# Kernel optimization log

Measured on AMD Instinct MI355X. Metric: run time of the kernel, lower is better.

The kernel has to match this reference:

```python
import jax, jax.numpy as jnp
import numpy as np

# TT-matrix dense layer: y = relu(x @ M + b) where M is a TT-matrix with cores
# G_k of shape [r_{k-1}, m_k, n_k, r_k], M[i1..id, j1..jd] = G1[:,i1,j1,:] ... Gd[:,id,jd,:]

IN_DIMS = [8, 8, 8, 8]
OUT_DIMS = [8, 8, 8, 8]
RANKS = [1, 8, 8, 8, 1]
BATCH = 4096


def setup_inputs() -> dict:
    key = jax.random.key(0)
    ks = jax.random.split(key, 6)
    inp = {"x": jax.random.normal(ks[0], (BATCH, int(np.prod(IN_DIMS))), dtype=jnp.float32)}
    # glorot-ish scale for TT cores so that the reconstructed matrix has sane variance
    for k in range(4):
        shape = (RANKS[k], IN_DIMS[k], OUT_DIMS[k], RANKS[k + 1])
        scale = 0.3
        inp[f"core{k}"] = scale * jax.random.normal(ks[1 + k], shape, dtype=jnp.float32)
    inp["b"] = 0.1 * jnp.ones((int(np.prod(OUT_DIMS)),), dtype=jnp.float32)
    return inp


def _tt_matmul(x, cores):
    # x: [B, prod(m)], cores[k]: [r_{k-1}, m_k, n_k, r_k]
    B = x.shape[0]
    ms = [G.shape[1] for G in cores]
    # res: [a, r, m_k, t] with a = B * prod(n_done), t = prod(m_rest)
    res = x.reshape(B, 1, ms[0], -1)
    for k, G in enumerate(cores):
        a, _, _, t = res.shape
        n, r_next = G.shape[2], G.shape[3]
        # contract rank and current input mode: [a, n, r_next, t]
        res = jnp.einsum('aqmt,qmnr->anrt', res, G)
        m_next = ms[k + 1] if k + 1 < len(cores) else 1
        res = res.reshape(a * n, r_next, m_next, t // m_next)
    return res.reshape(B, -1)  # [B, prod(n)], big-endian output index order


def reference(x, core0, core1, core2, core3, b):
    y = _tt_matmul(x, [core0, core1, core2, core3])
    return jax.nn.relu(y + b)
```

## Files before the change

### kernel.cpp

```cpp
#include <hip/hip_runtime.h>
#include <hip/hip_bf16.h>
#include <stdint.h>

typedef short bf16x8 __attribute__((ext_vector_type(8)));
typedef float f32x4 __attribute__((ext_vector_type(4)));
typedef unsigned short u16;
typedef u16 ushort8 __attribute__((ext_vector_type(8)));

typedef __attribute__((address_space(3))) void lds_void;
typedef const __attribute__((address_space(1))) void gbl_void;

#define BAR() do { asm volatile("" ::: "memory"); __builtin_amdgcn_s_barrier(); asm volatile("" ::: "memory"); } while (0)
#define WAITV(N) asm volatile("s_waitcnt vmcnt(" #N ")" ::: "memory")

__device__ __forceinline__ u16 f2bf(float f) {
  uint32_t u = __builtin_bit_cast(uint32_t, f);
  u += 0x7fffu + ((u >> 16) & 1u);
  return (u16)(u >> 16);
}

__global__ __launch_bounds__(256) void cvt_x(const float* __restrict__ x,
                                             u16* __restrict__ xb) {
  const int i = (blockIdx.x * 256 + threadIdx.x) * 8;
  float4 a = *(const float4*)(x + i);
  float4 b = *(const float4*)(x + i + 4);
  ushort8 o;
  o[0] = f2bf(a.x); o[1] = f2bf(a.y); o[2] = f2bf(a.z); o[3] = f2bf(a.w);
  o[4] = f2bf(b.x); o[5] = f2bf(b.y); o[6] = f2bf(b.z); o[7] = f2bf(b.w);
  *(ushort8*)(xb + i) = o;
}

__global__ __launch_bounds__(256) void build_mt(
    const float* __restrict__ c0, const float* __restrict__ c1,
    const float* __restrict__ c2, const float* __restrict__ c3,
    u16* __restrict__ Mt) {
  const int bid = blockIdx.x;
  const int j1 = bid & 7, i1 = (bid >> 3) & 7, j0 = (bid >> 6) & 7, i0 = bid >> 9;
  const int t = threadIdx.x;
  __shared__ float v[512];
  __shared__ float g3[512];
  g3[t] = c3[t];
  g3[t + 256] = c3[t + 256];
  float w2[8];
#pragma unroll
  for (int r2 = 0; r2 < 8; ++r2) {
    float s = 0.f;
#pragma unroll
    for (int r1 = 0; r1 < 8; ++r1)
      s += c0[(i0 * 8 + j0) * 8 + r1] * c1[((r1 * 8 + i1) * 8 + j1) * 8 + r2];
    w2[r2] = s;
  }
#pragma unroll
  for (int e = t; e < 512; e += 256) {
    const int r3 = e & 7, j2 = (e >> 3) & 7, i2 = e >> 6;
    float s = 0.f;
#pragma unroll
    for (int r2 = 0; r2 < 8; ++r2)
      s += w2[r2] * c2[((r2 * 8 + i2) * 8 + j2) * 8 + r3];
    v[e] = s;
  }
  __syncthreads();
  const int jr = t >> 2, ic0 = (t & 3) * 16;
  const int j2 = jr >> 3, j3 = jr & 7;
  const size_t base =
      (size_t)(j0 * 512 + j1 * 64 + jr) * 4096 + (i0 * 512 + i1 * 64) + ic0;
  ushort8 o0, o1;
#pragma unroll
  for (int q = 0; q < 16; ++q) {
    const int ic = ic0 + q, i2 = ic >> 3, i3 = ic & 7;
    float s = 0.f;
#pragma unroll
    for (int r3 = 0; r3 < 8; ++r3)
      s += v[(i2 << 6) + (j2 << 3) + r3] * g3[(r3 << 6) + (i3 << 3) + j3];
    const u16 h = f2bf(s);
    if (q < 8) o0[q] = h; else o1[q - 8] = h;
  }
  *(ushort8*)(Mt + base) = o0;
  *(ushort8*)(Mt + base + 8) = o1;
}

__global__ __launch_bounds__(512, 2) void gemm_bias_relu(
    const u16* __restrict__ A, const u16* __restrict__ Bt,
    const float* __restrict__ bias, float* __restrict__ C) {
  constexpr int K = 4096, N = 4096, NT = 64;
  __shared__ __align__(16) char lds[131072];
  const int t = threadIdx.x;
  const int l = t & 63, w = t >> 6;
  const int wr = w >> 2, wc = w & 3;
  const int lr = l & 15, lk = l >> 4;
  const int bm = blockIdx.y, bn = blockIdx.x;

  const char* gA = (const char*)A + (size_t)bm * 256 * (K * 2);
  const char* gB = (const char*)Bt + (size_t)bn * 256 * (K * 2);
  const int srow = t >> 3;
  const int schunk = (t & 7) ^ (srow & 7);
  const int sgo = srow * (K * 2) + schunk * 16;
  const int sld = t * 16;

  const int axor = (lk ^ (lr & 7)) * 16;
  const int aoff0 = (wr * 128 + lr) * 128 + axor;
  const int aoff1 = aoff0 ^ 64;
  const int boff0 = 65536 + (wc * 64 + lr) * 128 + axor;
  const int boff1 = boff0 ^ 64;

  auto stA = [&](int p, int h, int kt) {
    const char* src = gA + (size_t)(h * 128) * (K * 2) + kt * 128 + sgo;
    char* dst = lds + p * 32768 + h * 16384 + sld;
    __builtin_amdgcn_global_load_lds((gbl_void*)src, (lds_void*)dst, 16, 0, 0);
    __builtin_amdgcn_global_load_lds((gbl_void*)(src + (size_t)64 * (K * 2)),
                                     (lds_void*)(dst + 8192), 16, 0, 0);
  };
  auto stB = [&](int p, int h, int kt) {
    const char* src = gB + (size_t)(h * 128) * (K * 2) + kt * 128 + sgo;
    char* dst = lds + 65536 + p * 32768 + h * 16384 + sld;
    __builtin_amdgcn_global_load_lds((gbl_void*)src, (lds_void*)dst, 16, 0, 0);
    __builtin_amdgcn_global_load_lds((gbl_void*)(src + (size_t)64 * (K * 2)),
                                     (lds_void*)(dst + 8192), 16, 0, 0);
  };
  auto rdA = [&](int p, int off, int m) -> bf16x8 {
    return *(const bf16x8*)(lds + p * 32768 + off + m * 2048);
  };
  auto rdB = [&](int p, int off, int n) -> bf16x8 {
    return *(const bf16x8*)(lds + p * 32768 + off + n * 2048);
  };

  bf16x8 aH0[8], aH1[8], bH0[4], bH1[4];
  f32x4 acc[8][4];
#pragma unroll
  for (int m = 0; m < 8; ++m)
#pragma unroll
    for (int n = 0; n < 4; ++n) acc[m][n] = f32x4{0.f, 0.f, 0.f, 0.f};

  auto rdAH = [&](bf16x8* d, int p, int mh) {
#pragma unroll
    for (int m2 = 0; m2 < 4; ++m2) {
      d[m2 * 2 + 0] = rdA(p, aoff0, mh * 4 + m2);
      d[m2 * 2 + 1] = rdA(p, aoff1, mh * 4 + m2);
    }
  };
  auto rdBH = [&](bf16x8* d, int p, int nh) {
#pragma unroll
    for (int n2 = 0; n2 < 2; ++n2) {
      d[n2 * 2 + 0] = rdB(p, boff0, nh * 2 + n2);
      d[n2 * 2 + 1] = rdB(p, boff1, nh * 2 + n2);
    }
  };
  auto quad = [&](int mh, int nh, bf16x8* aH, bf16x8* bH) {
    __builtin_amdgcn_s_setprio(1);
#pragma unroll
    for (int kk = 0; kk < 2; ++kk)
#pragma unroll
      for (int m2 = 0; m2 < 4; ++m2)
#pragma unroll
        for (int n2 = 0; n2 < 2; ++n2)
          acc[mh * 4 + m2][nh * 2 + n2] = __builtin_amdgcn_mfma_f32_16x16x32_bf16(
              aH[m2 * 2 + kk], bH[n2 * 2 + kk], acc[mh * 4 + m2][nh * 2 + n2], 0, 0, 0);
    __builtin_amdgcn_s_setprio(0);
  };

  stA(0, 0, 0); stA(0, 1, 0); stB(0, 0, 0); stB(0, 1, 0);
  stB(1, 0, 1); stB(1, 1, 1);
  WAITV(4);
  BAR();
  rdAH(aH0, 0, 0); rdBH(bH0, 0, 0);
  stA(1, 0, 1);
  BAR();

  for (int it = 0; it < NT / 2; ++it) {
    const int T = 2 * it;
    const int t2 = (T + 2 < NT) ? T + 2 : NT - 1;
    const int t3 = (T + 3 < NT) ? T + 3 : NT - 1;
    rdBH(bH1, 0, 1);
    quad(0, 0, aH0, bH0);
    stA(1, 1, T + 1);
    BAR();
    rdAH(aH1, 0, 1);
    quad(0, 1, aH0, bH1);
    stB(0, 0, t2);
    BAR();
    quad(1, 1, aH1, bH1);
    stB(0, 1, t2); stA(0, 0, t2);
    WAITV(6);
    BAR();
    rdAH(aH0, 1, 0);
    quad(1, 0, aH1, bH0);
    rdBH(bH0, 1, 0);
    stA(0, 1, t2);
    BAR();
    rdBH(bH1, 1, 1);
    quad(0, 0, aH0, bH0);
    BAR();
    rdAH(aH1, 1, 1);
    quad(0, 1, aH0, bH1);
    stB(1, 0, t3);
    BAR();
    quad(1, 1, aH1, bH1);
    stB(1, 1, t3);
    WAITV(4);
    BAR();
    rdAH(aH0, 0, 0);
    quad(1, 0, aH1, bH0);
    rdBH(bH0, 0, 0);
    stA(1, 0, t3);
    BAR();
  }
  WAITV(0);

  const int row0 = bm * 256 + wr * 128;
  const int col0 = bn * 256 + wc * 64;
#pragma unroll
  for (int n = 0; n < 4; ++n) {
    const int col = col0 + n * 16 + lr;
    const float bv = bias[col];
#pragma unroll
    for (int m = 0; m < 8; ++m) {
      const int r0 = row0 + m * 16 + lk * 4;
#pragma unroll
      for (int vv = 0; vv < 4; ++vv) {
        const float val = acc[m][n][vv] + bv;
        C[(size_t)(r0 + vv) * N + col] = val > 0.f ? val : 0.f;
      }
    }
  }
}

extern "C" void kernel_launch(void* const* d_in, const int* in_sizes, int n_in,
                              void* d_out, int out_size, void* d_ws, size_t ws_size,
                              hipStream_t stream) {
  const float* x  = (const float*)d_in[0];
  const float* c0 = (const float*)d_in[1];
  const float* c1 = (const float*)d_in[2];
  const float* c2 = (const float*)d_in[3];
  const float* c3 = (const float*)d_in[4];
  const float* b  = (const float*)d_in[5];
  float* out = (float*)d_out;

  u16* xb  = (u16*)d_ws;
  u16* mtb = xb + (size_t)4096 * 4096;

  cvt_x<<<dim3(16777216 / (256 * 8)), dim3(256), 0, stream>>>(x, xb);
  build_mt<<<dim3(4096), dim3(256), 0, stream>>>(c0, c1, c2, c3, mtb);
  gemm_bias_relu<<<dim3(16, 16), dim3(512), 0, stream>>>(xb, mtb, b, out);
}
```

Baseline: 138.5 us.

## Fuse fp32-to-bf16 conversion of x into GEMM A-tile loading

Removes the separate cvt_x kernel and its bf16 staging buffer. The GEMM now loads fp32 rows of x into registers, converts them with v_cvt_pk_bf16_f32, and writes swizzled bf16 into LDS, so the A-tile pipeline is rescheduled around register-staged loads. The aim is to save a full kernel pass over x (read fp32, write bf16, reread) and one launch. In exchange the GEMM reads twice as many A bytes, needs extra registers (launch bounds drop to one block per CU), and adds more LDS waits in the main loop.

```diff
diff --git a/kernel.cpp b/kernel.cpp
--- a/kernel.cpp
+++ b/kernel.cpp
@@ -4,6 +4,7 @@
 
 typedef short bf16x8 __attribute__((ext_vector_type(8)));
 typedef float f32x4 __attribute__((ext_vector_type(4)));
+typedef float f32v4 __attribute__((ext_vector_type(4)));
 typedef unsigned short u16;
 typedef u16 ushort8 __attribute__((ext_vector_type(8)));
 
@@ -12,22 +13,12 @@
 
 #define BAR() do { asm volatile("" ::: "memory"); __builtin_amdgcn_s_barrier(); asm volatile("" ::: "memory"); } while (0)
 #define WAITV(N) asm volatile("s_waitcnt vmcnt(" #N ")" ::: "memory")
+#define LGKM0() asm volatile("s_waitcnt lgkmcnt(0)" ::: "memory")
 
 __device__ __forceinline__ u16 f2bf(float f) {
   uint32_t u = __builtin_bit_cast(uint32_t, f);
   u += 0x7fffu + ((u >> 16) & 1u);
   return (u16)(u >> 16);
-}
-
-__global__ __launch_bounds__(256) void cvt_x(const float* __restrict__ x,
-                                             u16* __restrict__ xb) {
-  const int i = (blockIdx.x * 256 + threadIdx.x) * 8;
-  float4 a = *(const float4*)(x + i);
-  float4 b = *(const float4*)(x + i + 4);
-  ushort8 o;
-  o[0] = f2bf(a.x); o[1] = f2bf(a.y); o[2] = f2bf(a.z); o[3] = f2bf(a.w);
-  o[4] = f2bf(b.x); o[5] = f2bf(b.y); o[6] = f2bf(b.z); o[7] = f2bf(b.w);
-  *(ushort8*)(xb + i) = o;
 }
 
 __global__ __launch_bounds__(256) void build_mt(
@@ -79,8 +70,8 @@
   *(ushort8*)(Mt + base + 8) = o1;
 }
 
-__global__ __launch_bounds__(512, 2) void gemm_bias_relu(
-    const u16* __restrict__ A, const u16* __restrict__ Bt,
+__global__ __launch_bounds__(512, 1) void gemm_bias_relu(
+    const float* __restrict__ X, const u16* __restrict__ Bt,
     const float* __restrict__ bias, float* __restrict__ C) {
   constexpr int K = 4096, N = 4096, NT = 64;
   __shared__ __align__(16) char lds[131072];
@@ -90,12 +81,14 @@
   const int lr = l & 15, lk = l >> 4;
   const int bm = blockIdx.y, bn = blockIdx.x;
 
-  const char* gA = (const char*)A + (size_t)bm * 256 * (K * 2);
+  const float* gAf = X + (size_t)bm * 256 * K;
   const char* gB = (const char*)Bt + (size_t)bn * 256 * (K * 2);
   const int srow = t >> 3;
   const int schunk = (t & 7) ^ (srow & 7);
   const int sgo = srow * (K * 2) + schunk * 16;
   const int sld = t * 16;
+  const int ar = t >> 2;
+  const int aq = t & 3;
 
   const int axor = (lk ^ (lr & 7)) * 16;
   const int aoff0 = (wr * 128 + lr) * 128 + axor;
@@ -103,12 +96,22 @@
   const int boff0 = 65536 + (wc * 64 + lr) * 128 + axor;
   const int boff1 = boff0 ^ 64;
 
-  auto stA = [&](int p, int h, int kt) {
-    const char* src = gA + (size_t)(h * 128) * (K * 2) + kt * 128 + sgo;
-    char* dst = lds + p * 32768 + h * 16384 + sld;
-    __builtin_amdgcn_global_load_lds((gbl_void*)src, (lds_void*)dst, 16, 0, 0);
-    __builtin_amdgcn_global_load_lds((gbl_void*)(src + (size_t)64 * (K * 2)),
-                                     (lds_void*)(dst + 8192), 16, 0, 0);
+  auto aload = [&](f32v4* L, int h, int kt) {
+    const float* src = gAf + (size_t)(h * 128 + ar) * K + kt * 64 + aq * 16;
+#pragma unroll
+    for (int j = 0; j < 4; ++j) L[j] = *(const f32v4*)(src + j * 4);
+  };
+  auto awrite = [&](const f32v4* L, int p, int h) {
+    uint32_t d[8];
+#pragma unroll
+    for (int j = 0; j < 4; ++j) {
+      asm("v_cvt_pk_bf16_f32 %0, %1, %2" : "=v"(d[2 * j]) : "v"(L[j][0]), "v"(L[j][1]));
+      asm("v_cvt_pk_bf16_f32 %0, %1, %2" : "=v"(d[2 * j + 1]) : "v"(L[j][2]), "v"(L[j][3]));
+    }
+    char* base = lds + p * 32768 + h * 16384 + ar * 128;
+    const int s = ar & 7;
+    *(uint4*)(base + (((2 * aq) ^ s) * 16)) = make_uint4(d[0], d[1], d[2], d[3]);
+    *(uint4*)(base + (((2 * aq + 1) ^ s) * 16)) = make_uint4(d[4], d[5], d[6], d[7]);
   };
   auto stB = [&](int p, int h, int kt) {
     const char* src = gB + (size_t)(h * 128) * (K * 2) + kt * 128 + sgo;
@@ -124,7 +127,7 @@
     return *(const bf16x8*)(lds + p * 32768 + off + n * 2048);
   };
 
-  bf16x8 aH0[8], aH1[8], bH0[4], bH1[4];
+  bf16x8 aH0[8], aH1[8], b01[2][2], b23[2][2];
   f32x4 acc[8][4];
 #pragma unroll
   for (int m = 0; m < 8; ++m)
@@ -138,14 +141,14 @@
       d[m2 * 2 + 1] = rdA(p, aoff1, mh * 4 + m2);
     }
   };
-  auto rdBH = [&](bf16x8* d, int p, int nh) {
+  auto rdBH = [&](bf16x8 (*d)[2], int p, int nh) {
 #pragma unroll
     for (int n2 = 0; n2 < 2; ++n2) {
-      d[n2 * 2 + 0] = rdB(p, boff0, nh * 2 + n2);
-      d[n2 * 2 + 1] = rdB(p, boff1, nh * 2 + n2);
-    }
-  };
-  auto quad = [&](int mh, int nh, bf16x8* aH, bf16x8* bH) {
+      d[n2][0] = rdB(p, boff0, nh * 2 + n2);
+      d[n2][1] = rdB(p, boff1, nh * 2 + n2);
+    }
+  };
+  auto quad = [&](int mh, int nh, bf16x8* aH, bf16x8 (*bH)[2]) {
     __builtin_amdgcn_s_setprio(1);
 #pragma unroll
     for (int kk = 0; kk < 2; ++kk)
@@ -154,54 +157,65 @@
 #pragma unroll
         for (int n2 = 0; n2 < 2; ++n2)
           acc[mh * 4 + m2][nh * 2 + n2] = __builtin_amdgcn_mfma_f32_16x16x32_bf16(
-              aH[m2 * 2 + kk], bH[n2 * 2 + kk], acc[mh * 4 + m2][nh * 2 + n2], 0, 0, 0);
+              aH[m2 * 2 + kk], bH[n2][kk], acc[mh * 4 + m2][nh * 2 + n2], 0, 0, 0);
     __builtin_amdgcn_s_setprio(0);
   };
 
-  stA(0, 0, 0); stA(0, 1, 0); stB(0, 0, 0); stB(0, 1, 0);
-  stB(1, 0, 1); stB(1, 1, 1);
+  f32v4 L_p2[4], L_p4[4], L_p5[4], L_p1[4];
+
+  aload(L_p4, 0, 0); aload(L_p5, 1, 0); aload(L_p1, 0, 1); aload(L_p2, 1, 1);
+  stB(0, 0, 0); stB(0, 1, 0); stB(1, 0, 1); stB(1, 1, 1);
+  awrite(L_p4, 0, 0); awrite(L_p5, 0, 1); awrite(L_p1, 1, 0); awrite(L_p2, 1, 1);
+  LGKM0();
   WAITV(4);
   BAR();
-  rdAH(aH0, 0, 0); rdBH(bH0, 0, 0);
-  stA(1, 0, 1);
+  rdAH(aH0, 0, 0); rdBH(b01, 0, 0);
+  aload(L_p2, 1, 1);
   BAR();
 
   for (int it = 0; it < NT / 2; ++it) {
     const int T = 2 * it;
     const int t2 = (T + 2 < NT) ? T + 2 : NT - 1;
     const int t3 = (T + 3 < NT) ? T + 3 : NT - 1;
-    rdBH(bH1, 0, 1);
-    quad(0, 0, aH0, bH0);
-    stA(1, 1, T + 1);
+    rdBH(b23, 0, 1);
+    aload(L_p4, 0, t2);
+    awrite(L_p2, 1, 1);
+    quad(0, 0, aH0, b01);
+    LGKM0();
     BAR();
     rdAH(aH1, 0, 1);
-    quad(0, 1, aH0, bH1);
+    aload(L_p5, 1, t2);
     stB(0, 0, t2);
-    BAR();
-    quad(1, 1, aH1, bH1);
-    stB(0, 1, t2); stA(0, 0, t2);
-    WAITV(6);
+    quad(0, 1, aH0, b23);
+    BAR();
+    awrite(L_p4, 0, 0);
+    quad(1, 1, aH1, b23);
+    stB(0, 1, t2);
+    LGKM0();
     BAR();
     rdAH(aH0, 1, 0);
-    quad(1, 0, aH1, bH0);
-    rdBH(bH0, 1, 0);
-    stA(0, 1, t2);
-    BAR();
-    rdBH(bH1, 1, 1);
-    quad(0, 0, aH0, bH0);
+    awrite(L_p5, 0, 1);
+    quad(1, 0, aH1, b01);
+    rdBH(b01, 1, 0);
+    LGKM0();
+    BAR();
+    rdBH(b23, 1, 1);
+    quad(0, 0, aH0, b01);
     BAR();
     rdAH(aH1, 1, 1);
-    quad(0, 1, aH0, bH1);
+    aload(L_p1, 0, t3);
     stB(1, 0, t3);
-    BAR();
-    quad(1, 1, aH1, bH1);
+    quad(0, 1, aH0, b23);
+    BAR();
+    aload(L_p2, 1, t3);
+    quad(1, 1, aH1, b23);
     stB(1, 1, t3);
-    WAITV(4);
     BAR();
     rdAH(aH0, 0, 0);
-    quad(1, 0, aH1, bH0);
-    rdBH(bH0, 0, 0);
-    stA(1, 0, t3);
+    awrite(L_p1, 1, 0);
+    quad(1, 0, aH1, b01);
+    rdBH(b01, 0, 0);
+    LGKM0();
     BAR();
   }
   WAITV(0);
@@ -235,10 +249,8 @@
   const float* b  = (const float*)d_in[5];
   float* out = (float*)d_out;
 
-  u16* xb  = (u16*)d_ws;
-  u16* mtb = xb + (size_t)4096 * 4096;
-
-  cvt_x<<<dim3(16777216 / (256 * 8)), dim3(256), 0, stream>>>(x, xb);
+  u16* mtb = (u16*)d_ws;
+
   build_mt<<<dim3(4096), dim3(256), 0, stream>>>(c0, c1, c2, c3, mtb);
-  gemm_bias_relu<<<dim3(16, 16), dim3(512), 0, stream>>>(xb, mtb, b, out);
-}
+  gemm_bias_relu<<<dim3(16, 16), dim3(512), 0, stream>>>(x, mtb, b, out);
+}
```

New measurement: 365.4 us. 2.64x slower.
